# Kernel optimization log

Measured on AMD Instinct MI355X. Metric: run time of the kernel, lower is better.

Reference implementation:

```python
import jax, jax.numpy as jnp
import numpy as np

N, T, D, H, E, ED = 4096, 16, 5, 128, 32768, 32

def _leaky(x):
    return jnp.where(x >= 0, x, 0.2 * x)

def _lstm(x, Wih, Whh, bih, bhh):
    # x: [N, T, D] -> hidden sequence [N, T, H]; PyTorch gate order i,f,g,o
    pre = jnp.einsum('ntd,gd->tng', x, Wih) + bih + bhh  # [T, N, 4H]
    Hd = Whh.shape[1]
    def step(carry, p):
        h, c = carry
        g = p + h @ Whh.T
        i, f, gg, o = jnp.split(g, 4, axis=-1)
        c = jax.nn.sigmoid(f) * c + jax.nn.sigmoid(i) * jnp.tanh(gg)
        h = jax.nn.sigmoid(o) * jnp.tanh(c)
        return (h, c), h
    z = jnp.zeros((x.shape[0], Hd), x.dtype)
    _, hs = jax.lax.scan(step, (z, z), pre)
    return jnp.swapaxes(hs, 0, 1)

def _sire(x, src, dst, efeat, Wq, bq, Wk, bk, We, be, Wr, br):
    # SIREConv with agg_type='sum': m = LeakyReLU(eq[dst]+ek[src]+e); sum over in-edges; then linear_relation
    eq = x @ Wq.T + bq            # [N, T, H]
    ek = x @ Wk.T + bk            # [N, T, H]
    e = efeat @ We.T + be         # [E, H]
    m = _leaky(eq[dst] + ek[src] + e[:, None, :])  # [E, T, H]
    ft = jax.ops.segment_sum(m, dst, num_segments=x.shape[0])  # [N, T, H]
    return ft @ Wr.T + br

def _forward(stock_features, srcs, dsts, efeats, sire_ps, lstm_p, attn_p, mlp_p):
    sf = stock_features / jnp.mean(stock_features, axis=1, keepdims=True)
    sr = _lstm(sf, *lstm_p)  # [N, T, H]
    outs = [sr]
    for s, d, ef, p in zip(srcs, dsts, efeats, sire_ps):
        outs.append(_sire(sr, s, d, ef, *p))
    cat = jnp.concatenate(outs, axis=-1)  # [N, T, 4H]
    aw = jax.nn.softmax(cat @ attn_p[0].T + attn_p[1], axis=-2)  # softmax over time
    pooled = jnp.sum(cat * aw, axis=-2)   # [N, 4H]
    W1, b1, W2, b2 = mlp_p
    h = _leaky(pooled @ W1.T + b1)
    out = _leaky(h @ W2.T + b2)           # [N, 1]
    return out / sf[:, -1, 0:1] - 1.0


def setup_inputs() -> dict:
    key = jax.random.key(0)
    ks = iter(jax.random.split(key, 64))
    def nrm(shape, s=0.05):
        return jax.random.normal(next(ks), shape, jnp.float32) * s
    inp = {}
    inp['stock_features'] = jax.random.uniform(next(ks), (N, T, D), jnp.float32) + 0.5
    for g in ['wiki', 'industry', 'corr']:
        inp[g + '_src'] = jax.random.randint(next(ks), (E,), 0, N, jnp.int32)
        inp[g + '_dst'] = jax.random.randint(next(ks), (E,), 0, N, jnp.int32)
        inp[g + '_efeat'] = nrm((E, ED), 1.0)
        inp[g + '_Wq'] = nrm((H, H)); inp[g + '_bq'] = nrm((H,))
        inp[g + '_Wk'] = nrm((H, H)); inp[g + '_bk'] = nrm((H,))
        inp[g + '_We'] = nrm((H, ED)); inp[g + '_be'] = nrm((H,))
        inp[g + '_Wr'] = nrm((H, H)); inp[g + '_br'] = nrm((H,))
    inp['lstm_Wih'] = nrm((4 * H, D)); inp['lstm_Whh'] = nrm((4 * H, H))
    inp['lstm_bih'] = nrm((4 * H,)); inp['lstm_bhh'] = nrm((4 * H,))
    inp['attn_W'] = nrm((1, 4 * H)); inp['attn_b'] = nrm((1,))
    inp['mlp_W1'] = nrm((H, 4 * H)); inp['mlp_b1'] = nrm((H,))
    inp['mlp_W2'] = nrm((1, H)); inp['mlp_b2'] = nrm((1,))
    return inp


def reference(stock_features, wiki_src, wiki_dst, wiki_efeat,
              wiki_Wq, wiki_bq, wiki_Wk, wiki_bk, wiki_We, wiki_be, wiki_Wr, wiki_br,
              industry_src, industry_dst, industry_efeat,
              industry_Wq, industry_bq, industry_Wk, industry_bk, industry_We, industry_be, industry_Wr, industry_br,
              corr_src, corr_dst, corr_efeat,
              corr_Wq, corr_bq, corr_Wk, corr_bk, corr_We, corr_be, corr_Wr, corr_br,
              lstm_Wih, lstm_Whh, lstm_bih, lstm_bhh,
              attn_W, attn_b, mlp_W1, mlp_b1, mlp_W2, mlp_b2):
    srcs = (wiki_src, industry_src, corr_src)
    dsts = (wiki_dst, industry_dst, corr_dst)
    efeats = (wiki_efeat, industry_efeat, corr_efeat)
    sire_ps = ((wiki_Wq, wiki_bq, wiki_Wk, wiki_bk, wiki_We, wiki_be, wiki_Wr, wiki_br),
               (industry_Wq, industry_bq, industry_Wk, industry_bk, industry_We, industry_be, industry_Wr, industry_br),
               (corr_Wq, corr_bq, corr_Wk, corr_bk, corr_We, corr_be, corr_Wr, corr_br))
    return _forward(stock_features, srcs, dsts, efeats, sire_ps,
                    (lstm_Wih, lstm_Whh, lstm_bih, lstm_bhh),
                    (attn_W, attn_b), (mlp_W1, mlp_b1, mlp_W2, mlp_b2))
```

## Files before the change

kernel.cpp:

```cpp
#include <hip/hip_runtime.h>
#include <cstdint>
#include <cstddef>

#define NS 4096
#define TS 16
#define DF 5
#define HD 128
#define EE 32768
#define EDD 32

typedef _Float16 h16;
typedef __attribute__((ext_vector_type(8))) _Float16 f16x8;
typedef __attribute__((ext_vector_type(2))) __fp16 fp16x2_n;
typedef __attribute__((ext_vector_type(4))) float f32x4;

__device__ __forceinline__ float sigmoidf_(float x){ return 1.f/(1.f+__expf(-x)); }
__device__ __forceinline__ float tanhf_(float x){ return 1.f - 2.f/(1.f+__expf(2.f*x)); }
__device__ __forceinline__ float leaky_(float x){ return x >= 0.f ? x : 0.2f*x; }

__device__ __forceinline__ unsigned pkh(float a, float b){
  union { fp16x2_n h; unsigned u; } x;
  x.h = __builtin_amdgcn_cvt_pkrtz(a, b);
  return x.u;
}
__device__ __forceinline__ void unpkh(unsigned u, float& a, float& b){
  union { unsigned u; fp16x2_n h; } x; x.u = u;
  a = (float)x.h.x; b = (float)x.h.y;
}
__device__ __forceinline__ f16x8 ld_h8(const h16* p){
  union { uint4 u; f16x8 v; } x; x.u = *(const uint4*)p; return x.v;
}

template<int AH, int CH>
__device__ __forceinline__ void gemm_dev(const void* Av, int lda,
    const float* __restrict__ Bp, int ldb, const float* __restrict__ bp,
    void* Cv, int ldc, int K, int act, size_t m0,
    h16* Asb, h16* Bsb)
{
  int tid = threadIdx.x;
  int wv = tid>>6, lane = tid&63, lm = lane&15, lq = lane>>4;
  f32x4 acc[2][8];
  #pragma unroll
  for (int mt=0;mt<2;mt++)
    #pragma unroll
    for (int nt=0;nt<8;nt++)
      acc[mt][nt] = (f32x4){0.f,0.f,0.f,0.f};

  for (int k0=0; k0<K; k0+=32){
    if (AH){
      const h16* A = (const h16*)Av;
      #pragma unroll
      for (int rep=0;rep<2;rep++){
        int idx = tid + rep*256;
        int row = idx>>2, c8 = idx&3;
        *(uint4*)&Asb[row*40 + c8*8] = *(const uint4*)&A[(m0+row)*(size_t)lda + k0 + c8*8];
      }
    } else {
      const float* A = (const float*)Av;
      #pragma unroll
      for (int rep=0;rep<4;rep++){
        int idx = tid + rep*256;
        int row = idx>>3, c4 = idx&7;
        float4 a = *(const float4*)&A[(m0+row)*(size_t)lda + k0 + c4*4];
        *(uint2*)&Asb[row*40 + c4*4] = make_uint2(pkh(a.x,a.y), pkh(a.z,a.w));
      }
    }
    #pragma unroll
    for (int rep=0;rep<4;rep++){
      int idx = tid + rep*256;
      int row = idx>>3, c4 = idx&7;
      float4 b = *(const float4*)&Bp[(size_t)row*ldb + k0 + c4*4];
      *(uint2*)&Bsb[row*40 + c4*4] = make_uint2(pkh(b.x,b.y), pkh(b.z,b.w));
    }
    __syncthreads();
    f16x8 afr[2], bfr[8];
    #pragma unroll
    for (int mt=0;mt<2;mt++)
      afr[mt] = ld_h8(&Asb[(wv*32 + mt*16 + lm)*40 + lq*8]);
    #pragma unroll
    for (int nt=0;nt<8;nt++)
      bfr[nt] = ld_h8(&Bsb[(nt*16 + lm)*40 + lq*8]);
    #pragma unroll
    for (int mt=0;mt<2;mt++)
      #pragma unroll
      for (int nt=0;nt<8;nt++)
        acc[mt][nt] = __builtin_amdgcn_mfma_f32_16x16x32_f16(afr[mt], bfr[nt], acc[mt][nt], 0,0,0);
    __syncthreads();
  }

  #pragma unroll
  for (int mt=0;mt<2;mt++){
    #pragma unroll
    for (int nt=0;nt<8;nt++){
      int col = nt*16 + lm;
      float bv = bp[col];
      #pragma unroll
      for (int i=0;i<4;i++){
        float o = acc[mt][nt][i] + bv;
        if (act) o = leaky_(o);
        size_t ridx = (m0 + wv*32 + mt*16 + lq*4 + i)*(size_t)ldc + col;
        if (CH) ((h16*)Cv)[ridx] = (h16)o;
        else    ((float*)Cv)[ridx] = o;
      }
    }
  }
}

__device__ void lstm8_dev(int blk, const float* __restrict__ sf,
                          const h16* __restrict__ WhhH,
                          const float* __restrict__ Wih, const float* __restrict__ bih,
                          const float* __restrict__ bhh, h16* __restrict__ cat,
                          char* smem)
{
  float* gates = (float*)smem;
  h16* hbuf = (h16*)(smem+16512);
  float* sfb = (float*)(smem+16512+2176);
  int tid = threadIdx.x;
  int n0 = blk*8;
  int wv = tid>>6, lane = tid&63, lm = lane&15, lq = lane>>4;

  f16x8 bfr[8][4];
  #pragma unroll
  for (int nt=0;nt<8;nt++){
    int g = wv*128 + nt*16 + lm;
    #pragma unroll
    for (int kt=0;kt<4;kt++)
      bfr[nt][kt] = *(const f16x8*)&WhhH[g*128 + kt*32 + lq*8];
  }

  int j = tid & 127;
  int rb = tid >> 7;
  float wih[4][5]; float bsum[4];
  #pragma unroll
  for (int gi=0; gi<4; gi++){
    int gc = gi*128 + j;
    #pragma unroll
    for (int d=0; d<5; d++) wih[gi][d] = Wih[gc*5+d];
    bsum[gi] = bih[gc] + bhh[gc];
  }
  float cst[4] = {0.f,0.f,0.f,0.f};

  for (int i=tid;i<544;i+=256) ((unsigned*)hbuf)[i] = 0;
  for (int i=tid;i<640;i+=256) sfb[i] = sf[(size_t)n0*80 + i];
  __syncthreads();

  f16x8 zf = {0,0,0,0,0,0,0,0};
  for (int t=0;t<16;t++){
    f16x8 af[4];
    #pragma unroll
    for (int kt=0;kt<4;kt++)
      af[kt] = (lm < 8) ? *(const f16x8*)&hbuf[lm*136 + kt*32 + lq*8] : zf;
    #pragma unroll
    for (int nt=0;nt<8;nt++){
      f32x4 acc = {0.f,0.f,0.f,0.f};
      #pragma unroll
      for (int kt=0;kt<4;kt++)
        acc = __builtin_amdgcn_mfma_f32_16x16x32_f16(af[kt], bfr[nt][kt], acc, 0,0,0);
      if (lq < 2){
        int col = wv*128 + nt*16 + lm;
        #pragma unroll
        for (int i=0;i<4;i++)
          gates[(lq*4+i)*516 + col] = acc[i];
      }
    }
    __syncthreads();
    #pragma unroll
    for (int q=0;q<4;q++){
      int r = rb + 2*q;
      const float* s = &sfb[r*80 + t*5];
      float pre[4];
      #pragma unroll
      for (int gi=0;gi<4;gi++){
        float a = bsum[gi];
        #pragma unroll
        for (int d=0;d<5;d++) a = fmaf(s[d], wih[gi][d], a);
        pre[gi] = a + gates[r*516 + gi*128 + j];
      }
      float iv = sigmoidf_(pre[0]);
      float fv = sigmoidf_(pre[1]);
      float gv = tanhf_(pre[2]);
      float ov = sigmoidf_(pre[3]);
      float c = fv*cst[q] + iv*gv;
      cst[q] = c;
      float h = ov*tanhf_(c);
      h16 hh = (h16)h;
      hbuf[r*136 + j] = hh;
      cat[(size_t)((n0+r)*16 + t)*512 + j] = hh;
    }
    __syncthreads();
  }
}

__global__ __launch_bounds__(256)
void k_prolog(const float* __restrict__ x, float* __restrict__ sf,
              const float* __restrict__ Whh, h16* __restrict__ whhH,
              int* __restrict__ cnt)
{
  int b = blockIdx.x, tid = threadIdx.x;
  if (b < 80){
    int id = b*256 + tid;
    if (id < NS*DF){
      int n = id / DF, d = id % DF;
      const float* xp = x + (size_t)n*TS*DF + d;
      float s = 0.f;
      #pragma unroll
      for (int t=0;t<TS;t++) s += xp[t*DF];
      float inv = (float)TS / s;
      float* sp = sf + (size_t)n*TS*DF + d;
      #pragma unroll
      for (int t=0;t<TS;t++) sp[t*DF] = xp[t*DF]*inv;
    }
  } else if (b < 336){
    int i = (b-80)*256 + tid;
    whhH[i] = (h16)Whh[i];
  } else {
    int i = (b-336)*256 + tid;
    cnt[i] = 0;
  }
}

struct M1 {
  const float *sf, *Wih, *bih, *bhh;
  const h16* WhhH;
  h16* cat;
  const float *ef[3]; const float *We[3]; const float *be[3];
  h16* eeb;
  const int* dst[3];
  int* cnt;
};
__global__ __launch_bounds__(256,2)
void k_mega1(M1 p)
{
  __shared__ __align__(16) char smem[21504];
  int b = blockIdx.x;
  if (b < 512){
    lstm8_dev(b, p.sf, p.WhhH, p.Wih, p.bih, p.bhh, p.cat, smem);
  } else if (b < 1280){
    int idx = b - 512;
    int proj = idx % 3, mt = idx / 3;
    h16* Asb = (h16*)smem;
    h16* Bsb = Asb + 128*40;
    gemm_dev<0,1>(p.ef[proj], 32, p.We[proj], 32, p.be[proj],
                  p.eeb + (size_t)proj*EE*128, 128, 32, 0, (size_t)mt*128, Asb, Bsb);
  } else {
    int idx = b - 1280;
    int g = idx >> 7, blk = idx & 127;
    int e = blk*256 + threadIdx.x;
    atomicAdd(&p.cnt[g*4096 + p.dst[g][e]], 1);
  }
}

__global__ __launch_bounds__(1024)
void k_scan(const int* __restrict__ cnt_, int* __restrict__ rs_, int* __restrict__ woff_){
  __shared__ int buf[1024];
  int g = blockIdx.x;
  const int* cnt = cnt_ + g*4096;
  int* rs = rs_ + g*4097;
  int* woff = woff_ + g*4096;
  int tid = threadIdx.x;
  int b = tid*4;
  int v0=cnt[b],v1=cnt[b+1],v2=cnt[b+2],v3=cnt[b+3];
  int s = v0+v1+v2+v3;
  buf[tid]=s;
  __syncthreads();
  for (int off=1; off<1024; off<<=1){
    int t = (tid>=off) ? buf[tid-off] : 0;
    __syncthreads();
    buf[tid] += t;
    __syncthreads();
  }
  int excl = buf[tid] - s;
  rs[b+0]=excl; woff[b+0]=excl; excl+=v0;
  rs[b+1]=excl; woff[b+1]=excl; excl+=v1;
  rs[b+2]=excl; woff[b+2]=excl; excl+=v2;
  rs[b+3]=excl; woff[b+3]=excl;
  if (tid==1023) rs[4096]=excl+v3;
}

struct M2 {
  const h16* cat;
  const float* W[6]; const float* bias[6];
  h16* eqk;
  const int* dst[3];
  int* woff; int* eidx;
};
__global__ __launch_bounds__(256)
void k_mega2(M2 p)
{
  __shared__ __align__(16) h16 Asb[128*40];
  __shared__ __align__(16) h16 Bsb[128*40];
  int b = blockIdx.x;
  if (b < 3072){
    int proj = b % 6, mt = b / 6;
    gemm_dev<1,1>(p.cat, 512, p.W[proj], 128, p.bias[proj],
                  p.eqk + (size_t)proj*NS*TS*128, 128, 128, 0, (size_t)mt*128, Asb, Bsb);
  } else {
    int idx = b - 3072;
    int g = idx >> 7, blk = idx & 127;
    int e = blk*256 + threadIdx.x;
    int pos = atomicAdd(&p.woff[g*4096 + p.dst[g][e]], 1);
    p.eidx[g*EE + pos] = e;
  }
}

struct P3 { const int* p[3]; };
__global__ __launch_bounds__(256)
void k_edge(const h16* __restrict__ eqk, const h16* __restrict__ eeb,
            P3 src, const int* __restrict__ rs_, const int* __restrict__ eidx_,
            h16* __restrict__ ft_)
{
  int n = blockIdx.x;
  int g = blockIdx.y;
  const h16* eqb = eqk + (size_t)(2*g)  *NS*TS*128;
  const h16* ekb = eqk + (size_t)(2*g+1)*NS*TS*128;
  const h16* eeg = eeb + (size_t)g*EE*128;
  h16* ft = ft_ + (size_t)g*NS*TS*128;
  const int* srcp = src.p[g];
  const int* rs = rs_ + g*4097;
  const int* eidx = eidx_ + g*EE;
  int tid = threadIdx.x;
  int t = tid>>4, hb = (tid&15)*8;
  size_t own = ((size_t)(n*16+t))*128 + hb;
  f16x8 eqv = ld_h8(&eqb[own]);
  const f16x8 c02 = {(h16)0.2f,(h16)0.2f,(h16)0.2f,(h16)0.2f,
                     (h16)0.2f,(h16)0.2f,(h16)0.2f,(h16)0.2f};
  float acc[8];
  #pragma unroll
  for (int j=0;j<8;j++) acc[j]=0.f;
  int i0 = rs[n], i1 = rs[n+1];
  for (int i=i0;i<i1;i++){
    int e = eidx[i];
    int s = srcp[e];
    f16x8 kv = ld_h8(&ekb[((size_t)(s*16+t))*128 + hb]);
    f16x8 ev = ld_h8(&eeg[(size_t)e*128 + hb]);
    f16x8 x = eqv + kv + ev;
    f16x8 lk = __builtin_elementwise_max(x, x*c02);
    #pragma unroll
    for (int j=0;j<8;j++) acc[j] += (float)lk[j];
  }
  uint4 o;
  o.x = pkh(acc[0],acc[1]); o.y = pkh(acc[2],acc[3]);
  o.z = pkh(acc[4],acc[5]); o.w = pkh(acc[6],acc[7]);
  *(uint4*)&ft[own] = o;
}

struct WrP {
  const h16* A[3];
  const float* B[3]; const float* bias[3];
  h16* C[3];
};
__global__ __launch_bounds__(256)
void k_wr(WrP p)
{
  __shared__ __align__(16) h16 Asb[128*40];
  __shared__ __align__(16) h16 Bsb[128*40];
  int proj = blockIdx.x;
  size_t m0 = (size_t)blockIdx.y * 128;
  gemm_dev<1,1>(p.A[proj], 128, p.B[proj], 128, p.bias[proj],
                p.C[proj], 512, 128, 0, m0, Asb, Bsb);
}

__global__ __launch_bounds__(256)
void k_attn(const h16* __restrict__ cat, const float* __restrict__ attnW,
            const float* __restrict__ attnB, h16* __restrict__ pooled)
{
  __shared__ h16 ct[16*512];
  __shared__ float sred[4][16];
  int n = blockIdx.x, tid = threadIdx.x;
  {
    const uint4* srcp = (const uint4*)(cat + (size_t)n*8192);
    uint4* dstp = (uint4*)ct;
    for (int i=tid;i<1024;i+=256) dstp[i] = srcp[i];
  }
  __syncthreads();
  int c0 = tid*2;
  float w0 = attnW[c0], w1 = attnW[c0+1];
  const unsigned* ctu = (const unsigned*)ct;
  float loc[16];
  #pragma unroll
  for (int t=0;t<16;t++){
    float a,b; unpkh(ctu[t*256 + tid], a, b);
    loc[t] = a*w0 + b*w1;
  }
  #pragma unroll
  for (int t=0;t<16;t++){
    float v = loc[t];
    for (int off=1; off<64; off<<=1) v += __shfl_xor(v, off, 64);
    loc[t]=v;
  }
  int wave = tid >> 6, lane = tid & 63;
  if (lane==0){
    #pragma unroll
    for (int t=0;t<16;t++) sred[wave][t]=loc[t];
  }
  __syncthreads();
  float s[16]; float m=-1e30f;
  float ab = attnB[0];
  #pragma unroll
  for (int t=0;t<16;t++){ s[t] = sred[0][t]+sred[1][t]+sred[2][t]+sred[3][t] + ab; m = fmaxf(m, s[t]); }
  float sum=0.f;
  #pragma unroll
  for (int t=0;t<16;t++){ s[t] = __expf(s[t]-m); sum += s[t]; }
  float inv = 1.f/sum;
  float p0=0.f,p1=0.f;
  #pragma unroll
  for (int t=0;t<16;t++){
    float a = s[t]*inv;
    float x,y; unpkh(ctu[t*256 + tid], x, y);
    p0 = fmaf(x, a, p0); p1 = fmaf(y, a, p1);
  }
  ((unsigned*)pooled)[(size_t)n*256 + tid] = pkh(p0,p1);
}

__global__ __launch_bounds__(256)
void k_mlp(const h16* __restrict__ pooled, const float* __restrict__ W1,
           const float* __restrict__ b1, float* __restrict__ hmlp)
{
  __shared__ __align__(16) h16 Asb[128*40];
  __shared__ __align__(16) h16 Bsb[128*40];
  gemm_dev<1,0>(pooled, 512, W1, 512, b1, hmlp, 128, 512, 1,
                (size_t)blockIdx.x*128, Asb, Bsb);
}

__global__ __launch_bounds__(256)
void k_final(const float* __restrict__ hmlp, const float* __restrict__ W2,
             const float* __restrict__ b2, const float* __restrict__ sf,
             float* __restrict__ out)
{
  int tid = threadIdx.x;
  int n = blockIdx.x*4 + (tid>>6);
  int lane = tid & 63;
  const float* hp = hmlp + (size_t)n*128;
  float v = hp[lane]*W2[lane] + hp[64+lane]*W2[64+lane];
  for (int off=1; off<64; off<<=1) v += __shfl_xor(v, off, 64);
  if (lane==0){
    float o = v + b2[0];
    o = leaky_(o);
    out[n] = o / sf[(size_t)n*80 + 75] - 1.f;
  }
}

extern "C" void kernel_launch(void* const* d_in, const int* in_sizes, int n_in,
                              void* d_out, int out_size, void* d_ws, size_t ws_size,
                              hipStream_t stream)
{
  const float* x    = (const float*)d_in[0];
  const float* Wih  = (const float*)d_in[34];
  const float* Whh  = (const float*)d_in[35];
  const float* bih  = (const float*)d_in[36];
  const float* bhh  = (const float*)d_in[37];
  const float* attnW= (const float*)d_in[38];
  const float* attnB= (const float*)d_in[39];
  const float* W1   = (const float*)d_in[40];
  const float* b1   = (const float*)d_in[41];
  const float* W2   = (const float*)d_in[42];
  const float* b2   = (const float*)d_in[43];

  char* w = (char*)d_ws;
  size_t o = 0;
  h16* cat    = (h16*)(w+o); o += (size_t)NS*TS*512*2;
  h16* eqk    = (h16*)(w+o); o += (size_t)6*NS*TS*128*2;
  h16* eeb    = (h16*)(w+o); o += (size_t)3*EE*128*2;
  h16* ft     = (h16*)(w+o); o += (size_t)3*NS*TS*128*2;
  h16* pooled = (h16*)(w+o); o += (size_t)NS*512*2;
  float* sf   = (float*)(w+o); o += (size_t)NS*TS*DF*4;
  float* hmlp = (float*)(w+o); o += (size_t)NS*HD*4;
  h16* whhH = (h16*)(w+o); o += (size_t)512*128*2;
  int* cnt  = (int*)(w+o); o += 3*4096*4;
  int* rs   = (int*)(w+o); o += 3*4097*4;
  int* woff = (int*)(w+o); o += 3*4096*4;
  int* eidx = (int*)(w+o); o += (size_t)3*EE*4;

  P3 srcs = {{ (const int*)d_in[1], (const int*)d_in[12], (const int*)d_in[23] }};

  k_prolog<<<384, 256, 0, stream>>>(x, sf, Whh, whhH, cnt);

  {
    M1 p;
    p.sf = sf; p.Wih = Wih; p.bih = bih; p.bhh = bhh;
    p.WhhH = whhH; p.cat = cat; p.eeb = eeb; p.cnt = cnt;
    for (int g=0; g<3; g++){
      int base = 1 + g*11;
      p.ef[g] = (const float*)d_in[base+2];
      p.We[g] = (const float*)d_in[base+7];
      p.be[g] = (const float*)d_in[base+8];
      p.dst[g] = (const int*)d_in[base+1];
    }
    k_mega1<<<1664, 256, 0, stream>>>(p);
  }

  k_scan<<<3, 1024, 0, stream>>>(cnt, rs, woff);

  {
    M2 p;
    p.cat = cat; p.eqk = eqk; p.woff = woff; p.eidx = eidx;
    for (int g=0; g<3; g++){
      int base = 1 + g*11;
      p.W[2*g]      = (const float*)d_in[base+3];
      p.bias[2*g]   = (const float*)d_in[base+4];
      p.W[2*g+1]    = (const float*)d_in[base+5];
      p.bias[2*g+1] = (const float*)d_in[base+6];
      p.dst[g] = (const int*)d_in[base+1];
    }
    k_mega2<<<3456, 256, 0, stream>>>(p);
  }

  k_edge<<<dim3(NS,3), 256, 0, stream>>>(eqk, eeb, srcs, rs, eidx, ft);

  {
    WrP p;
    for (int g=0; g<3; g++){
      int base = 1 + g*11;
      p.A[g]    = ft + (size_t)g*NS*TS*128;
      p.B[g]    = (const float*)d_in[base+9];
      p.bias[g] = (const float*)d_in[base+10];
      p.C[g]    = cat + (size_t)(1+g)*128;
    }
    k_wr<<<dim3(3,512), 256, 0, stream>>>(p);
  }

  k_attn<<<NS, 256, 0, stream>>>(cat, attnW, attnB, pooled);
  k_mlp<<<32, 256, 0, stream>>>(pooled, W1, b1, hmlp);
  k_final<<<NS/4, 256, 0, stream>>>(hmlp, W2, b2, sf, (float*)d_out);
}
```

Measured before the change: 380.4 us.

## Fuse attention pooling with MLP head, stage GEMM stores via LDS, cache edge indices

Merges the attention-pooling, MLP hidden GEMM and final projection kernels into one kernel that handles two stocks per block. The first MLP layer is now done with fp32 FMAs instead of MFMA, and the pooled and hidden intermediates no longer make a round trip through global memory. The fp16 GEMM epilogue now stages results in LDS and writes coalesced 16-byte rows instead of scattered 2-byte stores. The edge kernel preloads up to 64 edge and source indices into shared memory, and the prolog blocks are reordered. The trade-off is that each fused block rereads W1 from global memory (via cache) once per stock pair.

```diff
diff --git a/kernel.cpp b/kernel.cpp
--- a/kernel.cpp
+++ b/kernel.cpp
@@ -88,19 +88,47 @@
     __syncthreads();
   }
 
-  #pragma unroll
-  for (int mt=0;mt<2;mt++){
-    #pragma unroll
-    for (int nt=0;nt<8;nt++){
-      int col = nt*16 + lm;
-      float bv = bp[col];
-      #pragma unroll
-      for (int i=0;i<4;i++){
-        float o = acc[mt][nt][i] + bv;
-        if (act) o = leaky_(o);
-        size_t ridx = (m0 + wv*32 + mt*16 + lq*4 + i)*(size_t)ldc + col;
-        if (CH) ((h16*)Cv)[ridx] = (h16)o;
-        else    ((float*)Cv)[ridx] = o;
+  if (CH){
+    h16* lds = Asb;
+    h16* C = (h16*)Cv;
+    #pragma unroll
+    for (int mt=0;mt<2;mt++){
+      __syncthreads();
+      h16* lws = lds + wv*2176;
+      #pragma unroll
+      for (int nt=0;nt<8;nt++){
+        int col = nt*16 + lm;
+        float bv = bp[col];
+        #pragma unroll
+        for (int i=0;i<4;i++){
+          float o = acc[mt][nt][i] + bv;
+          if (act) o = leaky_(o);
+          lws[(lq*4+i)*136 + col] = (h16)o;
+        }
+      }
+      __syncthreads();
+      #pragma unroll
+      for (int it=0; it<4; it++){
+        int q = tid + it*256;
+        int rr = q>>4, cc = q&15;
+        int wvv = rr>>4, r = rr&15;
+        uint4 v = *(const uint4*)&lds[wvv*2176 + r*136 + cc*8];
+        *(uint4*)&C[(m0 + wvv*32 + mt*16 + r)*(size_t)ldc + cc*8] = v;
+      }
+    }
+  } else {
+    #pragma unroll
+    for (int mt=0;mt<2;mt++){
+      #pragma unroll
+      for (int nt=0;nt<8;nt++){
+        int col = nt*16 + lm;
+        float bv = bp[col];
+        #pragma unroll
+        for (int i=0;i<4;i++){
+          float o = acc[mt][nt][i] + bv;
+          if (act) o = leaky_(o);
+          ((float*)Cv)[(m0 + wv*32 + mt*16 + lq*4 + i)*(size_t)ldc + col] = o;
+        }
       }
     }
   }
@@ -197,8 +225,11 @@
               int* __restrict__ cnt)
 {
   int b = blockIdx.x, tid = threadIdx.x;
-  if (b < 80){
-    int id = b*256 + tid;
+  if (b < 48){
+    int i = b*256 + tid;
+    if (i < 3*4096) cnt[i] = 0;
+  } else if (b < 128){
+    int id = (b-48)*256 + tid;
     if (id < NS*DF){
       int n = id / DF, d = id % DF;
       const float* xp = x + (size_t)n*TS*DF + d;
@@ -210,12 +241,9 @@
       #pragma unroll
       for (int t=0;t<TS;t++) sp[t*DF] = xp[t*DF]*inv;
     }
-  } else if (b < 336){
-    int i = (b-80)*256 + tid;
+  } else {
+    int i = (b-128)*256 + tid;
     whhH[i] = (h16)Whh[i];
-  } else {
-    int i = (b-336)*256 + tid;
-    cnt[i] = 0;
   }
 }
 
@@ -309,6 +337,7 @@
             P3 src, const int* __restrict__ rs_, const int* __restrict__ eidx_,
             h16* __restrict__ ft_)
 {
+  __shared__ int sl_e[64], sl_s[64];
   int n = blockIdx.x;
   int g = blockIdx.y;
   const h16* eqb = eqk + (size_t)(2*g)  *NS*TS*128;
@@ -319,6 +348,13 @@
   const int* rs = rs_ + g*4097;
   const int* eidx = eidx_ + g*EE;
   int tid = threadIdx.x;
+  int i0 = rs[n], i1 = rs[n+1];
+  int ne = i1 - i0;
+  if (tid < 64 && tid < ne){
+    int e = eidx[i0 + tid];
+    sl_e[tid] = e;
+    sl_s[tid] = srcp[e];
+  }
   int t = tid>>4, hb = (tid&15)*8;
   size_t own = ((size_t)(n*16+t))*128 + hb;
   f16x8 eqv = ld_h8(&eqb[own]);
@@ -327,10 +363,11 @@
   float acc[8];
   #pragma unroll
   for (int j=0;j<8;j++) acc[j]=0.f;
-  int i0 = rs[n], i1 = rs[n+1];
-  for (int i=i0;i<i1;i++){
-    int e = eidx[i];
-    int s = srcp[e];
+  __syncthreads();
+  for (int i=0;i<ne;i++){
+    int e, s;
+    if (i < 64){ e = sl_e[i]; s = sl_s[i]; }
+    else       { e = eidx[i0+i]; s = srcp[e]; }
     f16x8 kv = ld_h8(&ekb[((size_t)(s*16+t))*128 + hb]);
     f16x8 ev = ld_h8(&eeg[(size_t)e*128 + hb]);
     f16x8 x = eqv + kv + ev;
@@ -362,81 +399,94 @@
 
 __global__ __launch_bounds__(256)
 void k_attn(const h16* __restrict__ cat, const float* __restrict__ attnW,
-            const float* __restrict__ attnB, h16* __restrict__ pooled)
-{
-  __shared__ h16 ct[16*512];
+            const float* __restrict__ attnB,
+            const float* __restrict__ W1, const float* __restrict__ b1,
+            const float* __restrict__ W2, const float* __restrict__ b2,
+            const float* __restrict__ sf, float* __restrict__ out)
+{
+  __shared__ h16 ct[2*16*512];
+  __shared__ float pool[2*516];
   __shared__ float sred[4][16];
-  int n = blockIdx.x, tid = threadIdx.x;
+  __shared__ float hred[2*128];
+  int nb = blockIdx.x*2, tid = threadIdx.x;
   {
-    const uint4* srcp = (const uint4*)(cat + (size_t)n*8192);
-    uint4* dstp = (uint4*)ct;
-    for (int i=tid;i<1024;i+=256) dstp[i] = srcp[i];
+    const uint4* srcp = (const uint4*)(cat + (size_t)nb*8192);
+    uint4* dst4 = (uint4*)ct;
+    for (int i=tid;i<2048;i+=256) dst4[i] = srcp[i];
   }
   __syncthreads();
   int c0 = tid*2;
   float w0 = attnW[c0], w1 = attnW[c0+1];
-  const unsigned* ctu = (const unsigned*)ct;
-  float loc[16];
-  #pragma unroll
-  for (int t=0;t<16;t++){
-    float a,b; unpkh(ctu[t*256 + tid], a, b);
-    loc[t] = a*w0 + b*w1;
-  }
-  #pragma unroll
-  for (int t=0;t<16;t++){
-    float v = loc[t];
+  float ab = attnB[0];
+  int wave = tid >> 6, lane = tid & 63;
+  for (int r=0;r<2;r++){
+    const unsigned* ctu = (const unsigned*)(ct + r*8192);
+    float loc[16];
+    #pragma unroll
+    for (int t=0;t<16;t++){
+      float a,b; unpkh(ctu[t*256 + tid], a, b);
+      loc[t] = a*w0 + b*w1;
+    }
+    #pragma unroll
+    for (int t=0;t<16;t++){
+      float v = loc[t];
+      for (int off=1; off<64; off<<=1) v += __shfl_xor(v, off, 64);
+      loc[t]=v;
+    }
+    if (lane==0){
+      #pragma unroll
+      for (int t=0;t<16;t++) sred[wave][t]=loc[t];
+    }
+    __syncthreads();
+    float s[16]; float m=-1e30f;
+    #pragma unroll
+    for (int t=0;t<16;t++){ s[t] = sred[0][t]+sred[1][t]+sred[2][t]+sred[3][t] + ab; m = fmaxf(m, s[t]); }
+    float sum=0.f;
+    #pragma unroll
+    for (int t=0;t<16;t++){ s[t] = __expf(s[t]-m); sum += s[t]; }
+    float inv = 1.f/sum;
+    float p0=0.f,p1=0.f;
+    #pragma unroll
+    for (int t=0;t<16;t++){
+      float a = s[t]*inv;
+      float x,y; unpkh(ctu[t*256 + tid], x, y);
+      p0 = fmaf(x, a, p0); p1 = fmaf(y, a, p1);
+    }
+    pool[r*516 + c0] = p0; pool[r*516 + c0 + 1] = p1;
+    __syncthreads();
+  }
+  int j = tid & 127, hf = tid >> 7;
+  float a2[2] = {0.f, 0.f};
+  const float* w1p = W1 + (size_t)j*512 + hf*256;
+  for (int k4=0; k4<256; k4+=4){
+    float4 wv4 = *(const float4*)&w1p[k4];
+    int kc = hf*256 + k4;
+    #pragma unroll
+    for (int r=0;r<2;r++){
+      float4 pv = *(const float4*)&pool[r*516 + kc];
+      a2[r] += pv.x*wv4.x + pv.y*wv4.y + pv.z*wv4.z + pv.w*wv4.w;
+    }
+  }
+  if (hf==1){
+    #pragma unroll
+    for (int r=0;r<2;r++) hred[r*128 + j] = a2[r];
+  }
+  __syncthreads();
+  if (hf==0){
+    float bj = b1[j];
+    #pragma unroll
+    for (int r=0;r<2;r++)
+      hred[r*128 + j] = leaky_(a2[r] + hred[r*128 + j] + bj);
+  }
+  __syncthreads();
+  if (wave < 2){
+    int r = wave;
+    float v = hred[r*128 + lane]*W2[lane] + hred[r*128 + 64 + lane]*W2[64+lane];
     for (int off=1; off<64; off<<=1) v += __shfl_xor(v, off, 64);
-    loc[t]=v;
-  }
-  int wave = tid >> 6, lane = tid & 63;
-  if (lane==0){
-    #pragma unroll
-    for (int t=0;t<16;t++) sred[wave][t]=loc[t];
-  }
-  __syncthreads();
-  float s[16]; float m=-1e30f;
-  float ab = attnB[0];
-  #pragma unroll
-  for (int t=0;t<16;t++){ s[t] = sred[0][t]+sred[1][t]+sred[2][t]+sred[3][t] + ab; m = fmaxf(m, s[t]); }
-  float sum=0.f;
-  #pragma unroll
-  for (int t=0;t<16;t++){ s[t] = __expf(s[t]-m); sum += s[t]; }
-  float inv = 1.f/sum;
-  float p0=0.f,p1=0.f;
-  #pragma unroll
-  for (int t=0;t<16;t++){
-    float a = s[t]*inv;
-    float x,y; unpkh(ctu[t*256 + tid], x, y);
-    p0 = fmaf(x, a, p0); p1 = fmaf(y, a, p1);
-  }
-  ((unsigned*)pooled)[(size_t)n*256 + tid] = pkh(p0,p1);
-}
-
-__global__ __launch_bounds__(256)
-void k_mlp(const h16* __restrict__ pooled, const float* __restrict__ W1,
-           const float* __restrict__ b1, float* __restrict__ hmlp)
-{
-  __shared__ __align__(16) h16 Asb[128*40];
-  __shared__ __align__(16) h16 Bsb[128*40];
-  gemm_dev<1,0>(pooled, 512, W1, 512, b1, hmlp, 128, 512, 1,
-                (size_t)blockIdx.x*128, Asb, Bsb);
-}
-
-__global__ __launch_bounds__(256)
-void k_final(const float* __restrict__ hmlp, const float* __restrict__ W2,
-             const float* __restrict__ b2, const float* __restrict__ sf,
-             float* __restrict__ out)
-{
-  int tid = threadIdx.x;
-  int n = blockIdx.x*4 + (tid>>6);
-  int lane = tid & 63;
-  const float* hp = hmlp + (size_t)n*128;
-  float v = hp[lane]*W2[lane] + hp[64+lane]*W2[64+lane];
-  for (int off=1; off<64; off<<=1) v += __shfl_xor(v, off, 64);
-  if (lane==0){
-    float o = v + b2[0];
-    o = leaky_(o);
-    out[n] = o / sf[(size_t)n*80 + 75] - 1.f;
+    if (lane==0){
+      float o = leaky_(v + b2[0]);
+      out[nb+r] = o / sf[(size_t)(nb+r)*80 + 75] - 1.f;
+    }
   }
 }
 
@@ -462,9 +512,7 @@
   h16* eqk    = (h16*)(w+o); o += (size_t)6*NS*TS*128*2;
   h16* eeb    = (h16*)(w+o); o += (size_t)3*EE*128*2;
   h16* ft     = (h16*)(w+o); o += (size_t)3*NS*TS*128*2;
-  h16* pooled = (h16*)(w+o); o += (size_t)NS*512*2;
   float* sf   = (float*)(w+o); o += (size_t)NS*TS*DF*4;
-  float* hmlp = (float*)(w+o); o += (size_t)NS*HD*4;
   h16* whhH = (h16*)(w+o); o += (size_t)512*128*2;
   int* cnt  = (int*)(w+o); o += 3*4096*4;
   int* rs   = (int*)(w+o); o += 3*4097*4;
@@ -519,7 +567,5 @@
     k_wr<<<dim3(3,512), 256, 0, stream>>>(p);
   }
 
-  k_attn<<<NS, 256, 0, stream>>>(cat, attnW, attnB, pooled);
-  k_mlp<<<32, 256, 0, stream>>>(pooled, W1, b1, hmlp);
-  k_final<<<NS/4, 256, 0, stream>>>(hmlp, W2, b2, sf, (float*)d_out);
-}
+  k_attn<<<NS/2, 256, 0, stream>>>(cat, attnW, attnB, W1, b1, W2, b2, sf, (float*)d_out);
+}
```

New measurement: 419.0 us. 1.1x slower.
